# Performance work log

Measured on AMD Instinct MI355X. Metric: run time of the kernel, lower is better.

Reference implementation:

```python
import jax, jax.numpy as jnp
import numpy as np

# pywt 'db4' decomposition filters (mode='symmetric' is pywt's default)
DEC_LO = jnp.array([-0.010597401784997278, 0.032883011666982945, 0.030841381835986965,
                    -0.18703481171888114, -0.02798376941698385, 0.6308807679295904,
                    0.7148465705525415, 0.23037781330885523], dtype=jnp.float32)
DEC_HI = jnp.array([-0.23037781330885523, 0.7148465705525415, -0.6308807679295904,
                    -0.02798376941698385, 0.18703481171888114, 0.030841381835986965,
                    -0.032883011666982945, -0.010597401784997278], dtype=jnp.float32)


def _dwt_level(x):
    """Single-level DWT matching pywt.dwt(sig, 'db4', mode='symmetric').

    x: (N, L) -> (cA, cD), each (N, (L + 7) // 2).
    pywt extends the signal symmetrically by F-1 samples on each side, performs
    true convolution with the decomposition filter, and keeps odd output indices.
    Dropping the first padded sample lets a stride-2 VALID conv pick exactly those.
    """
    F = DEC_LO.shape[0]  # 8
    xp = jnp.pad(x, ((0, 0), (F - 1, F - 1)), mode='symmetric')[:, 1:]
    lhs = xp[:, None, :]  # (N, 1, Lp)

    def conv(filt):
        # lax conv is cross-correlation; flip filter for true convolution.
        rhs = filt[::-1][None, None, :]  # (1, 1, F)
        return jax.lax.conv_general_dilated(lhs, rhs, (2,), 'VALID')[:, 0, :]

    return conv(DEC_LO), conv(DEC_HI)


def setup_inputs() -> dict:
    key = jax.random.key(0)
    x = jax.random.normal(key, (8, 16384, 256), dtype=jnp.float32)
    return {"x": x}


def reference(x):
    B, S, C = x.shape
    sig = x.transpose(0, 2, 1).reshape(B * C, S)  # one 1D signal per (batch, channel)
    cA1, cD1 = _dwt_level(sig)   # level 1: lengths (S+7)//2
    cA2, cD2 = _dwt_level(cA1)   # level 2

    def unflat(t):
        return t.reshape(B, C, -1).transpose(0, 2, 1)  # (B, L, C)

    # pywt.wavedec(level=2) -> [cA2, cD2, cD1]; module maps: high=cD1, mid=cD2, low=cA2
    return unflat(cD1), unflat(cD2), unflat(cA2)
```

## Files before the change

kernel.cpp:

```cpp
#include <hip/hip_runtime.h>

#define B_N    8
#define S_LEN  16384
#define C_CH   256
#define CV     64
#define L1_LEN 8195
#define L2_LEN 4101
#define T2S    8
#define TILE   32
#define NTILES 129

typedef float v4 __attribute__((ext_vector_type(4)));

__device__ __forceinline__ int refl(int n, int L) {
  n = (n < 0) ? (-n - 1) : n;
  n = (n >= L) ? (2 * L - 1 - n) : n;
  return n;
}

__device__ __forceinline__ v4 vfma(float s, v4 a, v4 c) {
  c.x = fmaf(s, a.x, c.x);
  c.y = fmaf(s, a.y, c.y);
  c.z = fmaf(s, a.z, c.z);
  c.w = fmaf(s, a.w, c.w);
  return c;
}

__device__ constexpr float RLO[8] = {
   0.23037781330885523f,  0.7148465705525415f,   0.6308807679295904f,
  -0.02798376941698385f, -0.18703481171888114f,  0.030841381835986965f,
   0.032883011666982945f, -0.010597401784997278f };
__device__ constexpr float RHI[8] = {
  -0.010597401784997278f, -0.032883011666982945f, 0.030841381835986965f,
   0.18703481171888114f,  -0.02798376941698385f,  -0.6308807679295904f,
   0.7148465705525415f,   -0.23037781330885523f };

__global__ __launch_bounds__(256, 2)
void dwt2_fused(const float* __restrict__ xg,
                float* __restrict__ d1g,
                float* __restrict__ d2g,
                float* __restrict__ a2g) {
  const int lane = threadIdx.x & 63;
  const int wv   = threadIdx.x >> 6;
  const int b    = blockIdx.y;
  const int a2w  = blockIdx.x * TILE + wv * T2S;
  if (a2w > 4096) return;

  const v4* __restrict__ xr  = (const v4*)xg + (size_t)b * S_LEN  * CV + lane;
  v4*       __restrict__ d1r = (v4*)d1g      + (size_t)b * L1_LEN * CV + lane;
  v4*       __restrict__ d2r = (v4*)d2g      + (size_t)b * L2_LEN * CV + lane;
  v4*       __restrict__ a2r = (v4*)a2g      + (size_t)b * L2_LEN * CV + lane;

  if (a2w >= 8 && a2w <= 4088) {
    v4 xw[8], aw[8];
    const int s0 = 4 * a2w - 18;
    #pragma unroll
    for (int k = 0; k < 8; ++k) xw[k] = xr[(s0 + k) * CV];

    #pragma unroll
    for (int p = 0; p < 6; ++p) {
      v4 a = {0.f, 0.f, 0.f, 0.f};
      #pragma unroll
      for (int k = 0; k < 8; ++k) a = vfma(RLO[k], xw[k], a);
      aw[p] = a;
      #pragma unroll
      for (int k = 0; k < 6; ++k) xw[k] = xw[k + 2];
      xw[6] = xr[(s0 + 8 + 2 * p) * CV];
      xw[7] = xr[(s0 + 9 + 2 * p) * CV];
    }

    int i1 = 2 * a2w;
    #pragma unroll
    for (int t = 0; t < T2S; ++t) {
      v4 a0 = {0.f,0.f,0.f,0.f}, d0 = {0.f,0.f,0.f,0.f};
      #pragma unroll
      for (int k = 0; k < 8; ++k) {
        a0 = vfma(RLO[k], xw[k], a0);
        d0 = vfma(RHI[k], xw[k], d0);
      }
      __builtin_nontemporal_store(d0, &d1r[i1 * CV]);

      #pragma unroll
      for (int k = 0; k < 6; ++k) xw[k] = xw[k + 2];
      xw[6] = xr[(2 * i1 + 2) * CV];
      xw[7] = xr[(2 * i1 + 3) * CV];

      v4 a1 = {0.f,0.f,0.f,0.f}, dv = {0.f,0.f,0.f,0.f};
      #pragma unroll
      for (int k = 0; k < 8; ++k) {
        a1 = vfma(RLO[k], xw[k], a1);
        dv = vfma(RHI[k], xw[k], dv);
      }
      __builtin_nontemporal_store(dv, &d1r[(i1 + 1) * CV]);

      if (t + 1 < T2S) {
        #pragma unroll
        for (int k = 0; k < 6; ++k) xw[k] = xw[k + 2];
        xw[6] = xr[(2 * i1 + 4) * CV];
        xw[7] = xr[(2 * i1 + 5) * CV];
      }

      aw[6] = a0; aw[7] = a1;
      v4 ca = {0.f,0.f,0.f,0.f}, cd = {0.f,0.f,0.f,0.f};
      #pragma unroll
      for (int k = 0; k < 8; ++k) {
        ca = vfma(RLO[k], aw[k], ca);
        cd = vfma(RHI[k], aw[k], cd);
      }
      const int i2 = a2w + t;
      __builtin_nontemporal_store(ca, &a2r[i2 * CV]);
      __builtin_nontemporal_store(cd, &d2r[i2 * CV]);
      #pragma unroll
      for (int k = 0; k < 6; ++k) aw[k] = aw[k + 2];

      i1 += 2;
    }
    return;
  }

  const int i1_0 = 2 * a2w;
  const int i1_e = min(2 * a2w + 2 * T2S, L1_LEN);
  for (int i1 = i1_0; i1 < i1_e; ++i1) {
    v4 d = {0.f,0.f,0.f,0.f};
    #pragma unroll
    for (int k = 0; k < 8; ++k)
      d = vfma(RHI[k], xr[refl(2 * i1 - 6 + k, S_LEN) * CV], d);
    __builtin_nontemporal_store(d, &d1r[i1 * CV]);
  }
  const int i2_e = min(a2w + T2S, L2_LEN);
  for (int i2 = a2w; i2 < i2_e; ++i2) {
    v4 ca = {0.f,0.f,0.f,0.f}, cd = {0.f,0.f,0.f,0.f};
    #pragma unroll
    for (int k = 0; k < 8; ++k) {
      const int m = refl(2 * i2 - 6 + k, L1_LEN);
      v4 a = {0.f,0.f,0.f,0.f};
      #pragma unroll
      for (int j = 0; j < 8; ++j)
        a = vfma(RLO[j], xr[refl(2 * m - 6 + j, S_LEN) * CV], a);
      ca = vfma(RLO[k], a, ca);
      cd = vfma(RHI[k], a, cd);
    }
    __builtin_nontemporal_store(ca, &a2r[i2 * CV]);
    __builtin_nontemporal_store(cd, &d2r[i2 * CV]);
  }
}

extern "C" void kernel_launch(void* const* d_in, const int* in_sizes, int n_in,
                              void* d_out, int out_size, void* d_ws, size_t ws_size,
                              hipStream_t stream) {
  const float* x = (const float*)d_in[0];
  float* out = (float*)d_out;
  float* d1 = out;
  float* d2 = d1 + (size_t)B_N * L1_LEN * C_CH;
  float* a2 = d2 + (size_t)B_N * L2_LEN * C_CH;
  dim3 grid(NTILES, B_N);
  dwt2_fused<<<grid, dim3(256), 0, stream>>>(x, d1, d2, a2);
}
```

Before: 257.1 us.

## Stage level-1 approximation coefficients in shared memory across waves

Replaces the per-wave register sliding window with a block-cooperative scheme. All four waves compute the level-1 approximation rows for a 16-output tile into LDS, with boundary reflection handled uniformly, then read them back for level 2. The boundary slow path goes away and occupancy is raised to 4 blocks per SM. In exchange, each x row feeding the level-1 halo is loaded 8 times per output instead of sliding, so global reads rise, and halo rows are recomputed between tiles.

```diff
diff --git a/kernel.cpp b/kernel.cpp
--- a/kernel.cpp
+++ b/kernel.cpp
@@ -6,9 +6,9 @@
 #define CV     64
 #define L1_LEN 8195
 #define L2_LEN 4101
-#define T2S    8
-#define TILE   32
-#define NTILES 129
+#define T2     16
+#define ROWS   (2*T2 + 8)
+#define NT2    257
 
 typedef float v4 __attribute__((ext_vector_type(4)));
 
@@ -35,113 +35,59 @@
    0.18703481171888114f,  -0.02798376941698385f,  -0.6308807679295904f,
    0.7148465705525415f,   -0.23037781330885523f };
 
-__global__ __launch_bounds__(256, 2)
+__global__ __launch_bounds__(256, 4)
 void dwt2_fused(const float* __restrict__ xg,
                 float* __restrict__ d1g,
                 float* __restrict__ d2g,
                 float* __restrict__ a2g) {
   const int lane = threadIdx.x & 63;
-  const int wv   = threadIdx.x >> 6;
+  const int w    = threadIdx.x >> 6;
   const int b    = blockIdx.y;
-  const int a2w  = blockIdx.x * TILE + wv * T2S;
-  if (a2w > 4096) return;
+  const int a    = blockIdx.x * T2;
+
+  __shared__ v4 s_a1[ROWS][64];
 
   const v4* __restrict__ xr  = (const v4*)xg + (size_t)b * S_LEN  * CV + lane;
   v4*       __restrict__ d1r = (v4*)d1g      + (size_t)b * L1_LEN * CV + lane;
   v4*       __restrict__ d2r = (v4*)d2g      + (size_t)b * L2_LEN * CV + lane;
   v4*       __restrict__ a2r = (v4*)a2g      + (size_t)b * L2_LEN * CV + lane;
 
-  if (a2w >= 8 && a2w <= 4088) {
-    v4 xw[8], aw[8];
-    const int s0 = 4 * a2w - 18;
-    #pragma unroll
-    for (int k = 0; k < 8; ++k) xw[k] = xr[(s0 + k) * CV];
-
-    #pragma unroll
-    for (int p = 0; p < 6; ++p) {
-      v4 a = {0.f, 0.f, 0.f, 0.f};
-      #pragma unroll
-      for (int k = 0; k < 8; ++k) a = vfma(RLO[k], xw[k], a);
-      aw[p] = a;
-      #pragma unroll
-      for (int k = 0; k < 6; ++k) xw[k] = xw[k + 2];
-      xw[6] = xr[(s0 + 8 + 2 * p) * CV];
-      xw[7] = xr[(s0 + 9 + 2 * p) * CV];
-    }
-
-    int i1 = 2 * a2w;
-    #pragma unroll
-    for (int t = 0; t < T2S; ++t) {
-      v4 a0 = {0.f,0.f,0.f,0.f}, d0 = {0.f,0.f,0.f,0.f};
-      #pragma unroll
-      for (int k = 0; k < 8; ++k) {
-        a0 = vfma(RLO[k], xw[k], a0);
-        d0 = vfma(RHI[k], xw[k], d0);
-      }
-      __builtin_nontemporal_store(d0, &d1r[i1 * CV]);
-
-      #pragma unroll
-      for (int k = 0; k < 6; ++k) xw[k] = xw[k + 2];
-      xw[6] = xr[(2 * i1 + 2) * CV];
-      xw[7] = xr[(2 * i1 + 3) * CV];
-
-      v4 a1 = {0.f,0.f,0.f,0.f}, dv = {0.f,0.f,0.f,0.f};
-      #pragma unroll
-      for (int k = 0; k < 8; ++k) {
-        a1 = vfma(RLO[k], xw[k], a1);
-        dv = vfma(RHI[k], xw[k], dv);
-      }
-      __builtin_nontemporal_store(dv, &d1r[(i1 + 1) * CV]);
-
-      if (t + 1 < T2S) {
-        #pragma unroll
-        for (int k = 0; k < 6; ++k) xw[k] = xw[k + 2];
-        xw[6] = xr[(2 * i1 + 4) * CV];
-        xw[7] = xr[(2 * i1 + 5) * CV];
-      }
-
-      aw[6] = a0; aw[7] = a1;
-      v4 ca = {0.f,0.f,0.f,0.f}, cd = {0.f,0.f,0.f,0.f};
-      #pragma unroll
-      for (int k = 0; k < 8; ++k) {
-        ca = vfma(RLO[k], aw[k], ca);
-        cd = vfma(RHI[k], aw[k], cd);
-      }
-      const int i2 = a2w + t;
-      __builtin_nontemporal_store(ca, &a2r[i2 * CV]);
-      __builtin_nontemporal_store(cd, &d2r[i2 * CV]);
-      #pragma unroll
-      for (int k = 0; k < 6; ++k) aw[k] = aw[k + 2];
-
-      i1 += 2;
-    }
-    return;
-  }
-
-  const int i1_0 = 2 * a2w;
-  const int i1_e = min(2 * a2w + 2 * T2S, L1_LEN);
-  for (int i1 = i1_0; i1 < i1_e; ++i1) {
-    v4 d = {0.f,0.f,0.f,0.f};
+  #pragma unroll 2
+  for (int j = 0; j < ROWS / 4; ++j) {
+    const int m   = 4 * j + w;
+    const int i1n = 2 * a - 6 + m;
+    const int i1  = refl(i1n, L1_LEN);
+    v4 xv[8];
     #pragma unroll
     for (int k = 0; k < 8; ++k)
-      d = vfma(RHI[k], xr[refl(2 * i1 - 6 + k, S_LEN) * CV], d);
-    __builtin_nontemporal_store(d, &d1r[i1 * CV]);
-  }
-  const int i2_e = min(a2w + T2S, L2_LEN);
-  for (int i2 = a2w; i2 < i2_e; ++i2) {
+      xv[k] = xr[(size_t)refl(2 * i1 - 6 + k, S_LEN) * CV];
     v4 ca = {0.f,0.f,0.f,0.f}, cd = {0.f,0.f,0.f,0.f};
     #pragma unroll
     for (int k = 0; k < 8; ++k) {
-      const int m = refl(2 * i2 - 6 + k, L1_LEN);
-      v4 a = {0.f,0.f,0.f,0.f};
-      #pragma unroll
-      for (int j = 0; j < 8; ++j)
-        a = vfma(RLO[j], xr[refl(2 * m - 6 + j, S_LEN) * CV], a);
-      ca = vfma(RLO[k], a, ca);
-      cd = vfma(RHI[k], a, cd);
+      ca = vfma(RLO[k], xv[k], ca);
+      cd = vfma(RHI[k], xv[k], cd);
     }
-    __builtin_nontemporal_store(ca, &a2r[i2 * CV]);
-    __builtin_nontemporal_store(cd, &d2r[i2 * CV]);
+    s_a1[m][lane] = ca;
+    if (m >= 6 && m < 6 + 2 * T2 && i1n < L1_LEN)
+      __builtin_nontemporal_store(cd, &d1r[(size_t)i1n * CV]);
+  }
+  __syncthreads();
+
+  #pragma unroll
+  for (int j2 = 0; j2 < 4; ++j2) {
+    const int io = 4 * w + j2;
+    const int i2 = a + io;
+    v4 ca = {0.f,0.f,0.f,0.f}, cd = {0.f,0.f,0.f,0.f};
+    #pragma unroll
+    for (int k = 0; k < 8; ++k) {
+      const v4 av = s_a1[2 * io + k][lane];
+      ca = vfma(RLO[k], av, ca);
+      cd = vfma(RHI[k], av, cd);
+    }
+    if (i2 < L2_LEN) {
+      __builtin_nontemporal_store(ca, &a2r[(size_t)i2 * CV]);
+      __builtin_nontemporal_store(cd, &d2r[(size_t)i2 * CV]);
+    }
   }
 }
 
@@ -153,6 +99,6 @@
   float* d1 = out;
   float* d2 = d1 + (size_t)B_N * L1_LEN * C_CH;
   float* a2 = d2 + (size_t)B_N * L2_LEN * C_CH;
-  dim3 grid(NTILES, B_N);
+  dim3 grid(NT2, B_N);
   dwt2_fused<<<grid, dim3(256), 0, stream>>>(x, d1, d2, a2);
 }
```

New measurement: 250.6 us. 2.5% less time.
